# Kernel tuning notes

Hardware: AMD Instinct MI355X
Metric: run time of the kernel (lower is better)

Reference implementation:

```python
import jax, jax.numpy as jnp
import numpy as np
from jax import lax

B = 64          # graphs per batch
N0 = 1024       # nodes per graph (equal-sized graphs -> static topk shapes)
DEG = 16        # avg degree
E = B * N0 * DEG
D_IN, D_H, D_OUT = 100, 128, 256
RATIO, EPS = 0.5, 1e-5


def _seg_sum(v, idx, n):
    return jax.ops.segment_sum(v, idx, num_segments=n)


def _gcn(x, src, dst, w_e, W, b, n):
    h = x @ W
    deg = 1.0 + _seg_sum(w_e, dst, n)          # +1 for self-loop
    dinv = lax.rsqrt(deg)
    norm = (dinv[src] * dinv[dst] * w_e)[:, None]
    return _seg_sum(h[src] * norm, dst, n) + h / deg[:, None] + b


def _graphnorm(x, w, bias, ms, nb, k):
    # PyG GraphNorm: per-graph mean/var with learnable mean_scale
    xg = x.reshape(nb, k, -1)
    mean = xg.mean(1, keepdims=True)
    sub = xg - ms * mean
    var = (sub * sub).mean(1, keepdims=True)
    return (w * sub * lax.rsqrt(var + EPS) + bias).reshape(nb * k, -1)


def _topk(x, src, dst, emask, p, nb, n_per):
    # TopKPooling (min_score=None): score = tanh(x.p/||p||), keep top ceil(r*n)
    k = int(np.ceil(RATIO * n_per))
    score = jnp.tanh((x @ p) / jnp.linalg.norm(p))
    vals, idx = lax.top_k(score.reshape(nb, n_per), k)            # [nb, k]
    perm = (idx + (jnp.arange(nb) * n_per)[:, None]).reshape(-1)
    x_new = x[perm] * vals.reshape(-1)[:, None]
    mapping = jnp.full((nb * n_per,), -1, jnp.int32).at[perm].set(
        jnp.arange(nb * k, dtype=jnp.int32))
    ns, nd = mapping[src], mapping[dst]
    valid = emask & (ns >= 0) & (nd >= 0)   # filter_adj as a persistent mask
    return x_new, jnp.where(valid, ns, 0), jnp.where(valid, nd, 0), valid, k


def _forward(x, edge_index, W1, b1, W2, b2, W3, b3,
             gn1_w, gn1_b, gn1_ms, gn2_w, gn2_b, gn2_ms,
             gn3_w, gn3_b, gn3_ms, p1, p2, p3):
    src, dst = edge_index[0], edge_index[1]
    emask = jnp.ones(src.shape, bool)
    Ws, bs = (W1, W2, W3), (b1, b2, b3)
    gw = (gn1_w, gn2_w, gn3_w)
    gb = (gn1_b, gn2_b, gn3_b)
    gm = (gn1_ms, gn2_ms, gn3_ms)
    ps = (p1, p2, p3)
    n_per = N0
    for i in range(3):
        n = B * n_per
        x = _gcn(x, src, dst, emask.astype(x.dtype), Ws[i], bs[i], n)
        x = _graphnorm(x, gw[i], gb[i], gm[i], B, n_per)
        x = jax.nn.relu(x)              # dropout: identity in eval mode
        x, src, dst, emask, n_per = _topk(x, src, dst, emask, ps[i], B, n_per)
    xg = x.reshape(B, n_per, D_OUT)
    # global mean/max pool then concat -> [B, 2*D_OUT]
    return jnp.concatenate([xg.mean(1), xg.max(1)], axis=1)


def setup_inputs():
    key = jax.random.key(0)
    ks = jax.random.split(key, 20)
    x = jax.random.normal(ks[0], (B * N0, D_IN), jnp.float32)
    # random edges within each graph, then offset by graph base index
    e = jax.random.randint(ks[1], (2, B, N0 * DEG), 0, N0, jnp.int32)
    edge_index = (e + (jnp.arange(B, dtype=jnp.int32) * N0)[None, :, None]).reshape(2, -1)
    batch = jnp.repeat(jnp.arange(B, dtype=jnp.int32), N0)
    inp = dict(x=x, edge_index=edge_index, batch=batch)
    dims = [(D_IN, D_H), (D_H, D_H), (D_H, D_OUT)]
    for i, (di, do) in enumerate(dims, 1):
        inp[f"W{i}"] = jax.random.normal(ks[1 + i], (di, do), jnp.float32) / np.sqrt(di)
        inp[f"b{i}"] = jnp.zeros((do,), jnp.float32)
        inp[f"gn{i}_w"] = jnp.ones((do,), jnp.float32)
        inp[f"gn{i}_b"] = jnp.zeros((do,), jnp.float32)
        inp[f"gn{i}_ms"] = jnp.ones((do,), jnp.float32)
        inp[f"p{i}"] = jax.random.normal(ks[10 + i], (do,), jnp.float32)
    return inp


def reference(x, edge_index, batch, W1, b1, W2, b2, W3, b3,
              gn1_w, gn1_b, gn1_ms, gn2_w, gn2_b, gn2_ms,
              gn3_w, gn3_b, gn3_ms, p1, p2, p3):
    del batch  # equal-sized graphs: grouping is encoded by constants B, N0
    return _forward(x, edge_index, W1, b1, W2, b2, W3, b3,
                    gn1_w, gn1_b, gn1_ms, gn2_w, gn2_b, gn2_ms,
                    gn3_w, gn3_b, gn3_ms, p1, p2, p3)
```

## Files before the change

kernel.cpp:

```cpp
#include <hip/hip_runtime.h>

#define GN_EPS 1e-5f

constexpr int NB   = 64;
constexpr int EPG  = 16384;
constexpr int ETOT = NB * EPG;
constexpr int NTOT = 64 * 1024;

__global__ void cmap_init_kernel(int* __restrict__ cmap) {
    int i = blockIdx.x * blockDim.x + threadIdx.x;
    if (i < NTOT) cmap[i] = i;
}

template <int NPG>
__global__ __launch_bounds__(1024) void csr_build_kernel(
        const int* __restrict__ ei, const int* __restrict__ cmap,
        int* __restrict__ cnt, int* __restrict__ offs, float* __restrict__ dinv,
        int* __restrict__ csr_src) {
    __shared__ int lcnt[NPG];
    __shared__ int wsum[16];
    constexpr int NW = NPG / 64;
    const int g = blockIdx.x;
    const int t = threadIdx.x;
    const int ebase = g * EPG;
    constexpr int EPT = EPG / 1024;

    for (int i = t; i < NPG; i += 1024) lcnt[i] = 0;
    __syncthreads();

    int ms_[EPT], md_[EPT];
#pragma unroll
    for (int i = 0; i < EPT; i++) {
        int e = ebase + t + i * 1024;
        int s = cmap[ei[e]];
        int d = cmap[ei[ETOT + e]];
        bool ok = (s >= 0) && (d >= 0);
        ms_[i] = ok ? s : -1;
        md_[i] = ok ? (d - g * NPG) : 0;
        if (ok) atomicAdd(&lcnt[d - g * NPG], 1);
    }
    __syncthreads();

    const int lane = t & 63;
    const int wid  = t >> 6;
    int orig = (t < NPG) ? lcnt[t] : 0;
    int v = orig;
#pragma unroll
    for (int d = 1; d < 64; d <<= 1) {
        int u = __shfl_up(v, d);
        if (lane >= d) v += u;
    }
    if (lane == 63) wsum[wid] = v;
    __syncthreads();
    if (wid == 0) {
        int wv = (lane < NW) ? wsum[lane] : 0;
#pragma unroll
        for (int d = 1; d < 16; d <<= 1) {
            int u = __shfl_up(wv, d);
            if (lane >= d) wv += u;
        }
        if (lane < NW) wsum[lane] = wv;
    }
    __syncthreads();
    if (t < NPG) {
        int incl = v + ((wid > 0) ? wsum[wid - 1] : 0);
        int excl = incl - orig;
        cnt[g * NPG + t]  = orig;
        offs[g * NPG + t] = ebase + excl;
        dinv[g * NPG + t] = rsqrtf(1.0f + (float)orig);
        lcnt[t] = excl;
    }
    __syncthreads();

#pragma unroll
    for (int i = 0; i < EPT; i++) {
        if (ms_[i] >= 0) {
            int pos = atomicAdd(&lcnt[md_[i]], 1);
            csr_src[ebase + pos] = ms_[i];
        }
    }
}

template <int D4, int NPB>
__global__ __launch_bounds__(256) void gather_kernel(
        const float* __restrict__ x, const int* __restrict__ cnt,
        const int* __restrict__ offs, const float* __restrict__ dinv,
        const int* __restrict__ csr_src, float* __restrict__ z, int n, int bpg) {
    int bid   = blockIdx.x;
    int xcd   = bid & 7;
    int slot  = bid >> 3;
    int graph = xcd + 8 * (slot / bpg);
    int local = slot % bpg;
    int vb    = graph * bpg + local;

    int grp = threadIdx.x / D4;
    int f4  = threadIdx.x % D4;
    if (grp >= NPB) return;
    int v = vb * NPB + grp;
    if (v >= n) return;

    const float4* x4 = reinterpret_cast<const float4*>(x);
    int st = offs[v];
    int c  = cnt[v];
    float dv = dinv[v];
    float4 xv = x4[(size_t)v * D4 + f4];
    float4 acc = {xv.x * dv, xv.y * dv, xv.z * dv, xv.w * dv};
    int j = 0;
    for (; j + 4 <= c; j += 4) {
        int s0 = csr_src[st + j],     s1 = csr_src[st + j + 1];
        int s2 = csr_src[st + j + 2], s3 = csr_src[st + j + 3];
        float d0 = dinv[s0], d1 = dinv[s1], d2 = dinv[s2], d3 = dinv[s3];
        float4 h0 = x4[(size_t)s0 * D4 + f4];
        float4 h1 = x4[(size_t)s1 * D4 + f4];
        float4 h2 = x4[(size_t)s2 * D4 + f4];
        float4 h3 = x4[(size_t)s3 * D4 + f4];
        acc.x += h0.x * d0 + h1.x * d1 + h2.x * d2 + h3.x * d3;
        acc.y += h0.y * d0 + h1.y * d1 + h2.y * d2 + h3.y * d3;
        acc.z += h0.z * d0 + h1.z * d1 + h2.z * d2 + h3.z * d3;
        acc.w += h0.w * d0 + h1.w * d1 + h2.w * d2 + h3.w * d3;
    }
    for (; j < c; j++) {
        int s0 = csr_src[st + j];
        float d0 = dinv[s0];
        float4 h0 = x4[(size_t)s0 * D4 + f4];
        acc.x += h0.x * d0; acc.y += h0.y * d0; acc.z += h0.z * d0; acc.w += h0.w * d0;
    }
    float4 o = {acc.x * dv, acc.y * dv, acc.z * dv, acc.w * dv};
    reinterpret_cast<float4*>(z)[(size_t)v * D4 + f4] = o;
}

__global__ __launch_bounds__(256) void gemm128_kernel(const float* __restrict__ A,
                                                      const float* __restrict__ W,
                                                      const float* __restrict__ Bias,
                                                      float* __restrict__ C,
                                                      int M, int N, int K) {
    __shared__ float As[16][132];
    __shared__ float Bs[16][132];
    const int bm = blockIdx.x * 128;
    const int bn = blockIdx.y * 128;
    const int tid = threadIdx.x;
    const int tx = tid & 15, ty = tid >> 4;

    const int arow = tid >> 1;
    const int ak   = (tid & 1) * 8;
    const int brow = tid >> 5;
    const int bc4  = (tid & 31) * 4;

    float acc[2][2][4][4] = {};

    for (int k0 = 0; k0 < K; k0 += 16) {
        {
            const float* ap = A + (size_t)(bm + arow) * K + k0 + ak;
            float4 a0 = {0,0,0,0}, a1 = {0,0,0,0};
            if (k0 + ak < K)     a0 = *reinterpret_cast<const float4*>(ap);
            if (k0 + ak + 4 < K) a1 = *reinterpret_cast<const float4*>(ap + 4);
            As[ak + 0][arow] = a0.x; As[ak + 1][arow] = a0.y;
            As[ak + 2][arow] = a0.z; As[ak + 3][arow] = a0.w;
            As[ak + 4][arow] = a1.x; As[ak + 5][arow] = a1.y;
            As[ak + 6][arow] = a1.z; As[ak + 7][arow] = a1.w;
        }
        {
            float4 b0 = {0,0,0,0}, b1 = {0,0,0,0};
            if (k0 + brow < K)
                b0 = *reinterpret_cast<const float4*>(W + (size_t)(k0 + brow) * N + bn + bc4);
            if (k0 + brow + 8 < K)
                b1 = *reinterpret_cast<const float4*>(W + (size_t)(k0 + brow + 8) * N + bn + bc4);
            *reinterpret_cast<float4*>(&Bs[brow][bc4])     = b0;
            *reinterpret_cast<float4*>(&Bs[brow + 8][bc4]) = b1;
        }
        __syncthreads();
#pragma unroll
        for (int k = 0; k < 16; k++) {
            float4 a0 = *reinterpret_cast<const float4*>(&As[k][ty * 4]);
            float4 a1 = *reinterpret_cast<const float4*>(&As[k][64 + ty * 4]);
            float4 b0 = *reinterpret_cast<const float4*>(&Bs[k][tx * 4]);
            float4 b1 = *reinterpret_cast<const float4*>(&Bs[k][64 + tx * 4]);
            const float av[2][4] = {{a0.x, a0.y, a0.z, a0.w}, {a1.x, a1.y, a1.z, a1.w}};
            const float bv[2][4] = {{b0.x, b0.y, b0.z, b0.w}, {b1.x, b1.y, b1.z, b1.w}};
#pragma unroll
            for (int qi = 0; qi < 2; qi++)
#pragma unroll
                for (int qj = 0; qj < 2; qj++)
#pragma unroll
                    for (int i = 0; i < 4; i++)
#pragma unroll
                        for (int j = 0; j < 4; j++)
                            acc[qi][qj][i][j] += av[qi][i] * bv[qj][j];
        }
        __syncthreads();
    }
    float4 bb[2];
    bb[0] = *reinterpret_cast<const float4*>(&Bias[bn + tx * 4]);
    bb[1] = *reinterpret_cast<const float4*>(&Bias[bn + 64 + tx * 4]);
#pragma unroll
    for (int qi = 0; qi < 2; qi++)
#pragma unroll
        for (int i = 0; i < 4; i++) {
            int row = bm + qi * 64 + ty * 4 + i;
#pragma unroll
            for (int qj = 0; qj < 2; qj++) {
                float4 o = {acc[qi][qj][i][0] + bb[qj].x, acc[qi][qj][i][1] + bb[qj].y,
                            acc[qi][qj][i][2] + bb[qj].z, acc[qi][qj][i][3] + bb[qj].w};
                *reinterpret_cast<float4*>(&C[(size_t)row * N + bn + qj * 64 + tx * 4]) = o;
            }
        }
}

template <int D4>
__global__ __launch_bounds__(256) void gn_partial_kernel(
        const float* __restrict__ x, float* __restrict__ sum1, float* __restrict__ sum2,
        int n_per) {
    constexpr int GROUPS = 256 / D4;
    __shared__ float4 l1[256];
    __shared__ float4 l2[256];
    int g = blockIdx.x >> 3;
    int ch = blockIdx.x & 7;
    int f4 = threadIdx.x % D4;
    int grp = threadIdx.x / D4;
    int chunk = n_per / 8;
    int base = g * n_per + ch * chunk;
    const float4* x4 = reinterpret_cast<const float4*>(x);
    float4 s1 = {0.f, 0.f, 0.f, 0.f}, s2 = {0.f, 0.f, 0.f, 0.f};
    for (int i = grp; i < chunk; i += GROUPS) {
        float4 v = x4[(size_t)(base + i) * D4 + f4];
        s1.x += v.x; s1.y += v.y; s1.z += v.z; s1.w += v.w;
        s2.x += v.x * v.x; s2.y += v.y * v.y; s2.z += v.z * v.z; s2.w += v.w * v.w;
    }
    int t = threadIdx.x;
    l1[t] = s1; l2[t] = s2;
    __syncthreads();
    for (int str = 128; str >= D4; str >>= 1) {
        if (t < str) {
            float4 a = l1[t + str], b2 = l2[t + str];
            l1[t].x += a.x; l1[t].y += a.y; l1[t].z += a.z; l1[t].w += a.w;
            l2[t].x += b2.x; l2[t].y += b2.y; l2[t].z += b2.z; l2[t].w += b2.w;
        }
        __syncthreads();
    }
    if (t < D4) {
        size_t slot = (size_t)(g * 8 + ch) * (D4 * 4) + t * 4;
        *reinterpret_cast<float4*>(&sum1[slot]) = l1[t];
        *reinterpret_cast<float4*>(&sum2[slot]) = l2[t];
    }
}

__global__ void pnorm3_kernel(const float* __restrict__ p0, const float* __restrict__ p1,
                              const float* __restrict__ p2, int d0, int d1, int d2,
                              float* __restrict__ out) {
    __shared__ float red[256];
    const float* p = (blockIdx.x == 0) ? p0 : (blockIdx.x == 1) ? p1 : p2;
    int d          = (blockIdx.x == 0) ? d0 : (blockIdx.x == 1) ? d1 : d2;
    int t = threadIdx.x;
    float v = (t < d) ? p[t] : 0.0f;
    red[t] = v * v;
    __syncthreads();
    for (int s = 128; s; s >>= 1) {
        if (t < s) red[t] += red[t + s];
        __syncthreads();
    }
    if (t == 0) out[blockIdx.x] = 1.0f / sqrtf(red[0]);
}

template <int DO>
__global__ __launch_bounds__(256) void gn_apply_score_kernel(
        float* __restrict__ x, const float* __restrict__ sum1, const float* __restrict__ sum2,
        const float* __restrict__ ms, const float* __restrict__ w,
        const float* __restrict__ bias, const float* __restrict__ p,
        const float* __restrict__ pinv, float* __restrict__ score, int n_per) {
    constexpr int V = DO / 64;
    __shared__ float scm[DO];
    __shared__ float ssr[DO];
    int node = blockIdx.x * 4 + (threadIdx.x >> 6);
    int lane = threadIdx.x & 63;
    int g = node / n_per;
    float inv_n = 1.0f / (float)n_per;
    for (int f = threadIdx.x; f < DO; f += 256) {
        float s1 = 0.f, s2 = 0.f;
#pragma unroll
        for (int ch = 0; ch < 8; ch++) {
            s1 += sum1[(size_t)(g * 8 + ch) * DO + f];
            s2 += sum2[(size_t)(g * 8 + ch) * DO + f];
        }
        float mean = s1 * inv_n;
        float ex2  = s2 * inv_n;
        float m = ms[f];
        float var = ex2 - 2.f * m * mean * mean + m * m * mean * mean;
        scm[f] = m * mean;
        ssr[f] = w[f] * rsqrtf(var + GN_EPS);
    }
    __syncthreads();

    float*       xr = x + (size_t)node * DO + lane * V;
    const float* bb = bias + lane * V;
    const float* pp = p + lane * V;
    float dot = 0.f;
#pragma unroll
    for (int i = 0; i < V; i++) {
        int f = lane * V + i;
        float y = (xr[i] - scm[f]) * ssr[f] + bb[i];
        y = fmaxf(y, 0.0f);
        xr[i] = y;
        dot += y * pp[i];
    }
#pragma unroll
    for (int off = 32; off; off >>= 1) dot += __shfl_xor(dot, off);
    if (lane == 0) score[node] = tanhf(dot * pinv[0]);
}

template <int N, int K>
__global__ __launch_bounds__(1024) void topk_radix_kernel(
        const float* __restrict__ score, int* __restrict__ mapping,
        int* __restrict__ inv) {
    __shared__ int hist[256];
    __shared__ int sscan[N];
    __shared__ int sbyte, sneed;
    const int g = blockIdx.x;
    const int t = threadIdx.x;
    float sc = score[g * N + t];
    unsigned u = __float_as_uint(sc);
    unsigned key = (u & 0x80000000u) ? ~u : (u | 0x80000000u);

    unsigned prefix = 0;
    int need = K;
#pragma unroll
    for (int shift = 24; shift >= 0; shift -= 8) {
        if (t < 256) hist[t] = 0;
        __syncthreads();
        unsigned hm = (shift == 24) ? 0u : (0xFFFFFFFFu << (shift + 8));
        if ((key & hm) == (prefix & hm))
            atomicAdd(&hist[(key >> shift) & 255], 1);
        __syncthreads();
        if (t < 256) sscan[t] = hist[t];
        __syncthreads();
        for (int d = 1; d < 256; d <<= 1) {
            int x = (t < 256 && t + d < 256) ? sscan[t + d] : 0;
            __syncthreads();
            if (t < 256) sscan[t] += x;
            __syncthreads();
        }
        if (t < 256) {
            int ge  = sscan[t];
            int gt_ = (t + 1 < 256) ? sscan[t + 1] : 0;
            if (ge >= need && gt_ < need) { sbyte = t; sneed = need - gt_; }
        }
        __syncthreads();
        prefix |= ((unsigned)sbyte << shift);
        need = sneed;
        __syncthreads();
    }
    bool gt = key > prefix;
    bool eq = (key == prefix);
    sscan[t] = (gt ? (1 << 16) : 0) | (eq ? 1 : 0);
    __syncthreads();
    for (int d = 1; d < N; d <<= 1) {
        int x = (t >= d) ? sscan[t - d] : 0;
        __syncthreads();
        sscan[t] += x;
        __syncthreads();
    }
    int incl   = sscan[t];
    int gtrank = (incl >> 16) - (gt ? 1 : 0);
    int eqrank = (incl & 0xFFFF) - (eq ? 1 : 0);
    int cntGT  = K - need;
    bool sel = gt || (eq && (eqrank < need));
    int old_g = g * N + t;
    if (sel) {
        int slot = gt ? gtrank : (cntGT + eqrank);
        mapping[old_g] = g * K + slot;
        inv[g * K + slot] = old_g;
    } else {
        mapping[old_g] = -1;
    }
}

__global__ void permute_compose_kernel(const float* __restrict__ x, const int* __restrict__ inv,
                                       const float* __restrict__ score, float* __restrict__ xn,
                                       int total, int ldof4,
                                       int* __restrict__ cmap, const int* __restrict__ mapping) {
    int t = blockIdx.x * blockDim.x + threadIdx.x;
    if (t < total) {
        int node = t >> ldof4;
        int f4   = t & ((1 << ldof4) - 1);
        int dof4 = 1 << ldof4;
        int old = inv[node];
        float sc = score[old];
        float4 v = reinterpret_cast<const float4*>(x)[(size_t)old * dof4 + f4];
        float4 o = {v.x * sc, v.y * sc, v.z * sc, v.w * sc};
        reinterpret_cast<float4*>(xn)[t] = o;
    }
    if (t < NTOT) {
        int c = cmap[t];
        cmap[t] = (c >= 0) ? mapping[c] : -1;
    }
}

__global__ __launch_bounds__(1024) void pool_sel_kernel(const float* __restrict__ x,
                                                        const int* __restrict__ inv,
                                                        const float* __restrict__ score,
                                                        float* __restrict__ out) {
    __shared__ float ssum[1024];
    __shared__ float smax[1024];
    int g = blockIdx.x;
    int f = threadIdx.x & 255;
    int ch = threadIdx.x >> 8;
    float s = 0.f, mx = -INFINITY;
    for (int i = ch; i < 128; i += 4) {
        int old = inv[g * 128 + i];
        float sc = score[old];
        float v = x[(size_t)old * 256 + f] * sc;
        s += v;
        mx = fmaxf(mx, v);
    }
    ssum[threadIdx.x] = s;
    smax[threadIdx.x] = mx;
    __syncthreads();
    if (ch == 0) {
#pragma unroll
        for (int c = 1; c < 4; c++) {
            s  += ssum[f + c * 256];
            mx  = fmaxf(mx, smax[f + c * 256]);
        }
        out[g * 512 + f]       = s / 128.0f;
        out[g * 512 + 256 + f] = mx;
    }
}

static inline int cdiv_h(int a, int b) { return (a + b - 1) / b; }

extern "C" void kernel_launch(void* const* d_in, const int* in_sizes, int n_in,
                              void* d_out, int out_size, void* d_ws, size_t ws_size,
                              hipStream_t stream) {
    (void)in_sizes; (void)n_in; (void)out_size; (void)ws_size;

    const float* x_in = (const float*)d_in[0];
    const int*   ei   = (const int*)d_in[1];
    const float* Wm[3]  = {(const float*)d_in[3],  (const float*)d_in[9],  (const float*)d_in[15]};
    const float* bv[3]  = {(const float*)d_in[4],  (const float*)d_in[10], (const float*)d_in[16]};
    const float* gnw[3] = {(const float*)d_in[5],  (const float*)d_in[11], (const float*)d_in[17]};
    const float* gnb[3] = {(const float*)d_in[6],  (const float*)d_in[12], (const float*)d_in[18]};
    const float* gnm[3] = {(const float*)d_in[7],  (const float*)d_in[13], (const float*)d_in[19]};
    const float* pv[3]  = {(const float*)d_in[8],  (const float*)d_in[14], (const float*)d_in[20]};

    size_t off = 0;
    auto alloc = [&](size_t bytes) {
        void* p = (char*)d_ws + off;
        off += (bytes + 255) & ~(size_t)255;
        return p;
    };
    float* X1      = (float*)alloc((size_t)65536 * 128 * 4);
    float* Z       = (float*)alloc((size_t)65536 * 128 * 4);
    float* X2      = (float*)alloc((size_t)32768 * 128 * 4);
    int*   csr_src = (int*)alloc((size_t)ETOT * 4);
    int*   cmap    = (int*)alloc(NTOT * 4);
    int*   cnt     = (int*)alloc(65536 * 4);
    int*   offs    = (int*)alloc(65536 * 4);
    float* dinv    = (float*)alloc(65536 * 4);
    float* score   = (float*)alloc(65536 * 4);
    int*   mapping = (int*)alloc(65536 * 4);
    int*   inv     = (int*)alloc(32768 * 4);
    float* sum1    = (float*)alloc(64 * 8 * 256 * 4);
    float* sum2    = (float*)alloc(64 * 8 * 256 * 4);
    float* pinv    = (float*)alloc(256);

    const int nper[4] = {1024, 512, 256, 128};
    const int din[3]  = {100, 128, 128};
    const int dof[3]  = {128, 128, 256};

    cmap_init_kernel<<<NTOT / 256, 256, 0, stream>>>(cmap);
    pnorm3_kernel<<<3, 256, 0, stream>>>(pv[0], pv[1], pv[2], dof[0], dof[1], dof[2], pinv);

    for (int L = 0; L < 3; L++) {
        const int n    = NB * nper[L];
        const int k    = nper[L + 1];
        const int nn   = NB * k;
        const int D    = dof[L];
        const int dof4 = D / 4;
        const int ldof4 = (dof4 == 32) ? 5 : 6;
        const float* xin = (L == 0) ? x_in : X2;

        if (nper[L] == 1024)
            csr_build_kernel<1024><<<NB, 1024, 0, stream>>>(ei, cmap, cnt, offs, dinv, csr_src);
        else if (nper[L] == 512)
            csr_build_kernel<512><<<NB, 1024, 0, stream>>>(ei, cmap, cnt, offs, dinv, csr_src);
        else
            csr_build_kernel<256><<<NB, 1024, 0, stream>>>(ei, cmap, cnt, offs, dinv, csr_src);

        {
            const int NPB = 8;
            const int bpg = nper[L] / NPB;
            if (L == 0)
                gather_kernel<25, 8><<<n / NPB, 256, 0, stream>>>(xin, cnt, offs, dinv,
                                                                  csr_src, Z, n, bpg);
            else
                gather_kernel<32, 8><<<n / NPB, 256, 0, stream>>>(xin, cnt, offs, dinv,
                                                                  csr_src, Z, n, bpg);
        }

        gemm128_kernel<<<dim3(n / 128, D / 128), 256, 0, stream>>>(Z, Wm[L], bv[L], X1,
                                                                   n, D, din[L]);

        if (dof4 == 32)
            gn_partial_kernel<32><<<NB * 8, 256, 0, stream>>>(X1, sum1, sum2, nper[L]);
        else
            gn_partial_kernel<64><<<NB * 8, 256, 0, stream>>>(X1, sum1, sum2, nper[L]);

        if (D == 128)
            gn_apply_score_kernel<128><<<n / 4, 256, 0, stream>>>(X1, sum1, sum2, gnm[L],
                                                                  gnw[L], gnb[L], pv[L],
                                                                  pinv + L, score, nper[L]);
        else
            gn_apply_score_kernel<256><<<n / 4, 256, 0, stream>>>(X1, sum1, sum2, gnm[L],
                                                                  gnw[L], gnb[L], pv[L],
                                                                  pinv + L, score, nper[L]);

        if (nper[L] == 1024)
            topk_radix_kernel<1024, 512><<<NB, 1024, 0, stream>>>(score, mapping, inv);
        else if (nper[L] == 512)
            topk_radix_kernel<512, 256><<<NB, 512, 0, stream>>>(score, mapping, inv);
        else
            topk_radix_kernel<256, 128><<<NB, 256, 0, stream>>>(score, mapping, inv);

        if (L < 2) {
            int total = nn * dof4;
            permute_compose_kernel<<<cdiv_h(total, 256), 256, 0, stream>>>(
                X1, inv, score, X2, total, ldof4, cmap, mapping);
        } else {
            pool_sel_kernel<<<NB, 1024, 0, stream>>>(X1, inv, score, (float*)d_out);
        }
    }
}
```

Baseline: 311.9 us.

## Pack source dinv into CSR entries and remap gather to 8 lanes per node

The CSR build now stores each edge as an int2 holding the source index and its dinv value, read from shared memory, so the gather no longer does a dependent dinv lookup per edge. The gather kernel is restructured to 8 lanes per node, each handling up to 4 float4 columns, with 32 nodes per block and a 2-way edge unroll. This removes a random-access load per edge and raises memory-level parallelism per thread, at the cost of doubling CSR storage traffic and some idle lanes for the 25-float4 layer.

```diff
diff --git a/kernel.cpp b/kernel.cpp
--- a/kernel.cpp
+++ b/kernel.cpp
@@ -16,9 +16,10 @@
 __global__ __launch_bounds__(1024) void csr_build_kernel(
         const int* __restrict__ ei, const int* __restrict__ cmap,
         int* __restrict__ cnt, int* __restrict__ offs, float* __restrict__ dinv,
-        int* __restrict__ csr_src) {
-    __shared__ int lcnt[NPG];
-    __shared__ int wsum[16];
+        int2* __restrict__ csr_pack) {
+    __shared__ int   lcnt[NPG];
+    __shared__ float sdv[NPG];
+    __shared__ int   wsum[16];
     constexpr int NW = NPG / 64;
     const int g = blockIdx.x;
     const int t = threadIdx.x;
@@ -65,27 +66,33 @@
     if (t < NPG) {
         int incl = v + ((wid > 0) ? wsum[wid - 1] : 0);
         int excl = incl - orig;
+        float dv = rsqrtf(1.0f + (float)orig);
         cnt[g * NPG + t]  = orig;
         offs[g * NPG + t] = ebase + excl;
-        dinv[g * NPG + t] = rsqrtf(1.0f + (float)orig);
+        dinv[g * NPG + t] = dv;
+        sdv[t] = dv;
         lcnt[t] = excl;
     }
     __syncthreads();
 
 #pragma unroll
     for (int i = 0; i < EPT; i++) {
-        if (ms_[i] >= 0) {
+        int s = ms_[i];
+        if (s >= 0) {
             int pos = atomicAdd(&lcnt[md_[i]], 1);
-            csr_src[ebase + pos] = ms_[i];
-        }
-    }
-}
-
-template <int D4, int NPB>
+            csr_pack[ebase + pos] = make_int2(s, __float_as_int(sdv[s - g * NPG]));
+        }
+    }
+}
+
+template <int D4>
 __global__ __launch_bounds__(256) void gather_kernel(
         const float* __restrict__ x, const int* __restrict__ cnt,
         const int* __restrict__ offs, const float* __restrict__ dinv,
-        const int* __restrict__ csr_src, float* __restrict__ z, int n, int bpg) {
+        const int2* __restrict__ csr_pack, float* __restrict__ z, int n, int bpg) {
+    constexpr int GRP = 8;
+    constexpr int NPB = 256 / GRP;
+    constexpr int CPL = 4;
     int bid   = blockIdx.x;
     int xcd   = bid & 7;
     int slot  = bid >> 3;
@@ -93,9 +100,8 @@
     int local = slot % bpg;
     int vb    = graph * bpg + local;
 
-    int grp = threadIdx.x / D4;
-    int f4  = threadIdx.x % D4;
-    if (grp >= NPB) return;
+    int grp  = threadIdx.x / GRP;
+    int lane = threadIdx.x % GRP;
     int v = vb * NPB + grp;
     if (v >= n) return;
 
@@ -103,30 +109,63 @@
     int st = offs[v];
     int c  = cnt[v];
     float dv = dinv[v];
-    float4 xv = x4[(size_t)v * D4 + f4];
-    float4 acc = {xv.x * dv, xv.y * dv, xv.z * dv, xv.w * dv};
+
+    int f4_[CPL];
+    bool act[CPL];
+#pragma unroll
+    for (int i = 0; i < CPL; i++) {
+        f4_[i] = lane + GRP * i;
+        act[i] = f4_[i] < D4;
+    }
+
+    float4 acc[CPL];
+#pragma unroll
+    for (int i = 0; i < CPL; i++) {
+        if (act[i]) {
+            float4 xv = x4[(size_t)v * D4 + f4_[i]];
+            acc[i] = {xv.x * dv, xv.y * dv, xv.z * dv, xv.w * dv};
+        } else {
+            acc[i] = {0.f, 0.f, 0.f, 0.f};
+        }
+    }
+
     int j = 0;
-    for (; j + 4 <= c; j += 4) {
-        int s0 = csr_src[st + j],     s1 = csr_src[st + j + 1];
-        int s2 = csr_src[st + j + 2], s3 = csr_src[st + j + 3];
-        float d0 = dinv[s0], d1 = dinv[s1], d2 = dinv[s2], d3 = dinv[s3];
-        float4 h0 = x4[(size_t)s0 * D4 + f4];
-        float4 h1 = x4[(size_t)s1 * D4 + f4];
-        float4 h2 = x4[(size_t)s2 * D4 + f4];
-        float4 h3 = x4[(size_t)s3 * D4 + f4];
-        acc.x += h0.x * d0 + h1.x * d1 + h2.x * d2 + h3.x * d3;
-        acc.y += h0.y * d0 + h1.y * d1 + h2.y * d2 + h3.y * d3;
-        acc.z += h0.z * d0 + h1.z * d1 + h2.z * d2 + h3.z * d3;
-        acc.w += h0.w * d0 + h1.w * d1 + h2.w * d2 + h3.w * d3;
-    }
-    for (; j < c; j++) {
-        int s0 = csr_src[st + j];
-        float d0 = dinv[s0];
-        float4 h0 = x4[(size_t)s0 * D4 + f4];
-        acc.x += h0.x * d0; acc.y += h0.y * d0; acc.z += h0.z * d0; acc.w += h0.w * d0;
-    }
-    float4 o = {acc.x * dv, acc.y * dv, acc.z * dv, acc.w * dv};
-    reinterpret_cast<float4*>(z)[(size_t)v * D4 + f4] = o;
+    for (; j + 2 <= c; j += 2) {
+        int2 p0 = csr_pack[st + j];
+        int2 p1 = csr_pack[st + j + 1];
+        float d0 = __int_as_float(p0.y);
+        float d1 = __int_as_float(p1.y);
+        size_t r0 = (size_t)p0.x * D4;
+        size_t r1 = (size_t)p1.x * D4;
+#pragma unroll
+        for (int i = 0; i < CPL; i++) {
+            if (!act[i]) continue;
+            float4 h0 = x4[r0 + f4_[i]];
+            float4 h1 = x4[r1 + f4_[i]];
+            acc[i].x += h0.x * d0 + h1.x * d1;
+            acc[i].y += h0.y * d0 + h1.y * d1;
+            acc[i].z += h0.z * d0 + h1.z * d1;
+            acc[i].w += h0.w * d0 + h1.w * d1;
+        }
+    }
+    if (j < c) {
+        int2 p0 = csr_pack[st + j];
+        float d0 = __int_as_float(p0.y);
+        size_t r0 = (size_t)p0.x * D4;
+#pragma unroll
+        for (int i = 0; i < CPL; i++) {
+            if (!act[i]) continue;
+            float4 h0 = x4[r0 + f4_[i]];
+            acc[i].x += h0.x * d0; acc[i].y += h0.y * d0;
+            acc[i].z += h0.z * d0; acc[i].w += h0.w * d0;
+        }
+    }
+#pragma unroll
+    for (int i = 0; i < CPL; i++) {
+        if (!act[i]) continue;
+        float4 o = {acc[i].x * dv, acc[i].y * dv, acc[i].z * dv, acc[i].w * dv};
+        reinterpret_cast<float4*>(z)[(size_t)v * D4 + f4_[i]] = o;
+    }
 }
 
 __global__ __launch_bounds__(256) void gemm128_kernel(const float* __restrict__ A,
@@ -450,7 +489,7 @@
     float* X1      = (float*)alloc((size_t)65536 * 128 * 4);
     float* Z       = (float*)alloc((size_t)65536 * 128 * 4);
     float* X2      = (float*)alloc((size_t)32768 * 128 * 4);
-    int*   csr_src = (int*)alloc((size_t)ETOT * 4);
+    int2*  csr_pack= (int2*)alloc((size_t)ETOT * 8);
     int*   cmap    = (int*)alloc(NTOT * 4);
     int*   cnt     = (int*)alloc(65536 * 4);
     int*   offs    = (int*)alloc(65536 * 4);
@@ -479,21 +518,21 @@
         const float* xin = (L == 0) ? x_in : X2;
 
         if (nper[L] == 1024)
-            csr_build_kernel<1024><<<NB, 1024, 0, stream>>>(ei, cmap, cnt, offs, dinv, csr_src);
+            csr_build_kernel<1024><<<NB, 1024, 0, stream>>>(ei, cmap, cnt, offs, dinv, csr_pack);
         else if (nper[L] == 512)
-            csr_build_kernel<512><<<NB, 1024, 0, stream>>>(ei, cmap, cnt, offs, dinv, csr_src);
+            csr_build_kernel<512><<<NB, 1024, 0, stream>>>(ei, cmap, cnt, offs, dinv, csr_pack);
         else
-            csr_build_kernel<256><<<NB, 1024, 0, stream>>>(ei, cmap, cnt, offs, dinv, csr_src);
+            csr_build_kernel<256><<<NB, 1024, 0, stream>>>(ei, cmap, cnt, offs, dinv, csr_pack);
 
         {
-            const int NPB = 8;
+            const int NPB = 32;
             const int bpg = nper[L] / NPB;
             if (L == 0)
-                gather_kernel<25, 8><<<n / NPB, 256, 0, stream>>>(xin, cnt, offs, dinv,
-                                                                  csr_src, Z, n, bpg);
+                gather_kernel<25><<<n / NPB, 256, 0, stream>>>(xin, cnt, offs, dinv,
+                                                               csr_pack, Z, n, bpg);
             else
-                gather_kernel<32, 8><<<n / NPB, 256, 0, stream>>>(xin, cnt, offs, dinv,
-                                                                  csr_src, Z, n, bpg);
+                gather_kernel<32><<<n / NPB, 256, 0, stream>>>(xin, cnt, offs, dinv,
+                                                               csr_pack, Z, n, bpg);
         }
 
         gemm128_kernel<<<dim3(n / 128, D / 128), 256, 0, stream>>>(Z, Wm[L], bv[L], X1,
```

Result: no change. 315.0 us (+1.0%).
